# Kernel tuning notes

Hardware: AMD Instinct MI355X
Metric: run time of the kernel (lower is better)

Reference implementation:

```python
import jax, jax.numpy as jnp
import numpy as np

N_NODES = 50000
N_EDGES = 800000   # avg degree ~16
IN_CH = 128
HID = 64


def setup_inputs() -> dict:
    key = jax.random.key(0)
    k0, k1, k2, k3 = jax.random.split(key, 4)
    x = jax.random.normal(k0, (N_NODES, IN_CH), dtype=jnp.float32)
    edge_index = jax.random.randint(k1, (2, N_EDGES), 0, N_NODES, dtype=jnp.int32)
    # Glorot-ish init like torch GCNConv
    W1 = jax.random.normal(k2, (IN_CH, HID), dtype=jnp.float32) / np.sqrt(IN_CH).astype(np.float32)
    b1 = jnp.zeros((HID,), dtype=jnp.float32)
    W2 = jax.random.normal(k3, (HID, HID), dtype=jnp.float32) / np.sqrt(HID).astype(np.float32)
    b2 = jnpp = jnp.zeros((HID,), dtype=jnp.float32)
    return {"x": x, "edge_index": edge_index, "W1": W1, "b1": b1, "W2": W2, "b2": b2}


def gcn_conv(x, src, dst, W, b, n):
    """GCNConv with self-loops already appended to (src, dst).
    out = D^{-1/2} (A + I) D^{-1/2} (x @ W) + b, symmetric normalization."""
    h = x @ W                                        # [N, out]
    deg = jax.ops.segment_sum(jnp.ones(src.shape, jnp.float32), dst, num_segments=n)
    dinv = jax.lax.rsqrt(jnp.maximum(deg, 1.0))      # deg >= 1 due to self-loops
    norm = dinv[src] * dinv[dst]                     # [E+N]
    msg = h[src] * norm[:, None]                     # gather + scale
    return jax.ops.segment_sum(msg, dst, num_segments=n) + b


def reference(x, edge_index, W1, b1, W2, b2):
    n = x.shape[0]
    loop = jnp.arange(n, dtype=edge_index.dtype)
    src = jnp.concatenate([edge_index[0], loop])     # add self-loops
    dst = jnp.concatenate([edge_index[1], loop])
    # encode: GCNConv -> ReLU -> GCNConv
    z = jax.nn.relu(gcn_conv(x, src, dst, W1, b1, n))
    z = gcn_conv(z, src, dst, W2, b2, n)
    # decode: gather endpoint embeddings, elementwise product, reduce over hidden
    return (z[edge_index[0]] * z[edge_index[1]]).sum(axis=1)   # [E]
```

## Files before the change

kernel.cpp:

```cpp
#include <hip/hip_runtime.h>
#include <hip/hip_fp16.h>

#define INCH 128
#define HIDC 64
#define CAP  64

typedef int            v4i __attribute__((ext_vector_type(4)));
typedef float          v4f __attribute__((ext_vector_type(4)));
typedef float          v2f __attribute__((ext_vector_type(2)));
typedef unsigned int   v4u __attribute__((ext_vector_type(4)));

__device__ inline float2 u2f(unsigned int u) {
    return __half22float2(__builtin_bit_cast(__half2, u));
}
__device__ inline unsigned int f2u(float a, float b) {
    __half2 h = __float22half2_rn(make_float2(a, b));
    return __builtin_bit_cast(unsigned int, h);
}

__global__ __launch_bounds__(128, 2) void build_gemm1_kernel(const int* __restrict__ src,
                                                             const int* __restrict__ dst,
                                                             int* __restrict__ count,
                                                             unsigned short* __restrict__ col,
                                                             const float* __restrict__ x,
                                                             const float* __restrict__ W,
                                                             __half* __restrict__ hs,
                                                             int E, int N, int EB) {
    int b = (int)blockIdx.x;
    if (b < EB) {
        int i8 = (b * 128 + (int)threadIdx.x) * 8;
        if (i8 + 7 < E) {
            v4i sa = __builtin_nontemporal_load((const v4i*)(src + i8));
            v4i sb = __builtin_nontemporal_load((const v4i*)(src + i8 + 4));
            v4i da = __builtin_nontemporal_load((const v4i*)(dst + i8));
            v4i db = __builtin_nontemporal_load((const v4i*)(dst + i8 + 4));
            int rs[8], ds[8], ss[8];
            ds[0]=da.x; ds[1]=da.y; ds[2]=da.z; ds[3]=da.w;
            ds[4]=db.x; ds[5]=db.y; ds[6]=db.z; ds[7]=db.w;
            ss[0]=sa.x; ss[1]=sa.y; ss[2]=sa.z; ss[3]=sa.w;
            ss[4]=sb.x; ss[5]=sb.y; ss[6]=sb.z; ss[7]=sb.w;
            #pragma unroll
            for (int k = 0; k < 8; ++k) rs[k] = atomicAdd(&count[ds[k]], 1);
            #pragma unroll
            for (int k = 0; k < 8; ++k)
                if (rs[k] < CAP) col[ds[k] * CAP + rs[k]] = (unsigned short)ss[k];
        } else {
            for (int i = i8; i < E; ++i) {
                int d = dst[i];
                int r = atomicAdd(&count[d], 1);
                if (r < CAP) col[d * CAP + r] = (unsigned short)src[i];
            }
        }
    } else {
        int nb = b - EB;
        int node = (nb >> 1) * 128 + (int)threadIdx.x;
        int ch0 = (nb & 1) * 32;
        if (node >= N) return;
        const float4* xr = (const float4*)(x + (size_t)node * INCH);
        float acc[32];
        #pragma unroll
        for (int c = 0; c < 32; ++c) acc[c] = 0.f;
        for (int kc = 0; kc < INCH / 4; ++kc) {
            float4 xk = xr[kc];
            const float* wr = W + (kc * 4) * HIDC + ch0;
            #pragma unroll
            for (int ch = 0; ch < 32; ++ch) acc[ch] = fmaf(xk.x, wr[ch], acc[ch]);
            #pragma unroll
            for (int ch = 0; ch < 32; ++ch) acc[ch] = fmaf(xk.y, wr[HIDC + ch], acc[ch]);
            #pragma unroll
            for (int ch = 0; ch < 32; ++ch) acc[ch] = fmaf(xk.z, wr[2 * HIDC + ch], acc[ch]);
            #pragma unroll
            for (int ch = 0; ch < 32; ++ch) acc[ch] = fmaf(xk.w, wr[3 * HIDC + ch], acc[ch]);
        }
        v4u hv[4];
        #pragma unroll
        for (int k = 0; k < 4; ++k) {
            #pragma unroll
            for (int e = 0; e < 4; ++e) {
                int c2 = k * 4 + e;
                hv[k][e] = f2u(acc[2 * c2], acc[2 * c2 + 1]);
            }
        }
        v4u* hr = (v4u*)(hs + (size_t)node * HIDC + ch0);
        #pragma unroll
        for (int k = 0; k < 4; ++k) hr[k] = hv[k];
    }
}

__global__ __launch_bounds__(256) void scale_kernel(const int* __restrict__ count,
                                                    __half* __restrict__ hs, int N) {
    int idx = (int)blockIdx.x * 256 + threadIdx.x;
    if (idx >= N * 8) return;
    int node = idx >> 3;
    float dn = rsqrtf((float)count[node] + 1.0f);
    v4u v = ((const v4u*)hs)[idx];
    v4u o;
    #pragma unroll
    for (int k = 0; k < 4; ++k) {
        float2 f = u2f(v[k]);
        o[k] = f2u(dn * f.x, dn * f.y);
    }
    ((v4u*)hs)[idx] = o;
}

__global__ __launch_bounds__(128, 2) void gemm2_kernel(const __half* __restrict__ agg1,
                                                       const float* __restrict__ W,
                                                       const int* __restrict__ count,
                                                       __half* __restrict__ hs, int N) {
    int node = (blockIdx.x >> 1) * 128 + threadIdx.x;
    int ch0 = (blockIdx.x & 1) * 32;
    if (node >= N) return;
    const v4u* ar = (const v4u*)(agg1 + (size_t)node * HIDC);
    float acc[32];
    #pragma unroll
    for (int c = 0; c < 32; ++c) acc[c] = 0.f;
    for (int kc = 0; kc < HIDC / 8; ++kc) {
        v4u av = ar[kc];
        #pragma unroll
        for (int k2 = 0; k2 < 4; ++k2) {
            float2 f = u2f(av[k2]);
            float v0 = fmaxf(f.x, 0.f);
            float v1 = fmaxf(f.y, 0.f);
            const float* wr = W + (kc * 8 + k2 * 2) * HIDC + ch0;
            #pragma unroll
            for (int ch = 0; ch < 32; ++ch) acc[ch] = fmaf(v0, wr[ch], acc[ch]);
            #pragma unroll
            for (int ch = 0; ch < 32; ++ch) acc[ch] = fmaf(v1, wr[HIDC + ch], acc[ch]);
        }
    }
    float dn = rsqrtf((float)count[node] + 1.0f);
    v4u hv[4];
    #pragma unroll
    for (int k = 0; k < 4; ++k) {
        #pragma unroll
        for (int e = 0; e < 4; ++e) {
            int c2 = k * 4 + e;
            hv[k][e] = f2u(dn * acc[2 * c2], dn * acc[2 * c2 + 1]);
        }
    }
    v4u* hr = (v4u*)(hs + (size_t)node * HIDC + ch0);
    #pragma unroll
    for (int k = 0; k < 4; ++k) hr[k] = hv[k];
}

__global__ __launch_bounds__(256) void aggregate_kernel(const int* __restrict__ count,
                                                        const unsigned short* __restrict__ col,
                                                        const __half* __restrict__ hs,
                                                        const float* __restrict__ bias,
                                                        __half* __restrict__ agg, int N) {
    int node = blockIdx.x * 8 + (threadIdx.x >> 5);
    int c2 = threadIdx.x & 31;
    if (node >= N) return;
    int cnt = count[node];
    int deg = cnt < CAP ? cnt : CAP;
    const unsigned int* h2p = (const unsigned int*)hs;
    float2 acc = u2f(h2p[(size_t)node * 32 + c2]);
    const unsigned short* row = col + (size_t)node * CAP;
    for (int jb = 0; jb < deg; jb += 16) {
        int s[16];
        unsigned int v[16];
        #pragma unroll
        for (int u = 0; u < 16; ++u) {
            int idx = jb + u;
            s[u] = row[idx < deg ? idx : jb];
        }
        #pragma unroll
        for (int u = 0; u < 16; ++u)
            v[u] = h2p[(size_t)s[u] * 32 + c2];
        #pragma unroll
        for (int u = 0; u < 16; ++u) {
            if (jb + u < deg) {
                float2 f = u2f(v[u]);
                acc.x += f.x; acc.y += f.y;
            }
        }
    }
    float dn = rsqrtf((float)cnt + 1.0f);
    float2 bb = *(const float2*)(bias + c2 * 2);
    ((unsigned int*)agg)[(size_t)node * 32 + c2] =
        f2u(fmaf(acc.x, dn, bb.x), fmaf(acc.y, dn, bb.y));
}

__global__ __launch_bounds__(256) void decode_kernel(const int* __restrict__ src,
                                                     const int* __restrict__ dst,
                                                     const __half* __restrict__ z,
                                                     float* __restrict__ out, int E) {
    long long tid = (long long)blockIdx.x * 256 + threadIdx.x;
    int g = (int)(tid >> 3);
    int q = threadIdx.x & 7;
    int e0 = g * 4;
    if (e0 >= E) return;
    const v4u* z8 = (const v4u*)z;
    bool full = (e0 + 3 < E);
    int s[4], d[4];
    if (full) {
        v4i sv = __builtin_nontemporal_load((const v4i*)(src + e0));
        v4i dv = __builtin_nontemporal_load((const v4i*)(dst + e0));
        s[0]=sv.x; s[1]=sv.y; s[2]=sv.z; s[3]=sv.w;
        d[0]=dv.x; d[1]=dv.y; d[2]=dv.z; d[3]=dv.w;
    } else {
        #pragma unroll
        for (int k = 0; k < 4; ++k) {
            int e = e0 + k < E ? e0 + k : e0;
            s[k] = src[e]; d[k] = dst[e];
        }
    }
    v4u a[4], b[4];
    #pragma unroll
    for (int k = 0; k < 4; ++k) a[k] = z8[(size_t)s[k] * 8 + q];
    #pragma unroll
    for (int k = 0; k < 4; ++k) b[k] = z8[(size_t)d[k] * 8 + q];
    float p[4];
    #pragma unroll
    for (int k = 0; k < 4; ++k) {
        float acc = 0.f;
        #pragma unroll
        for (int j = 0; j < 4; ++j) {
            float2 fa = u2f(a[k][j]);
            float2 fb = u2f(b[k][j]);
            acc = fmaf(fa.x, fb.x, acc);
            acc = fmaf(fa.y, fb.y, acc);
        }
        p[k] = acc;
    }
    #pragma unroll
    for (int m = 4; m; m >>= 1) {
        #pragma unroll
        for (int k = 0; k < 4; ++k) p[k] += __shfl_xor(p[k], m, 64);
    }
    if (q == 0) {
        if (full) {
            v4f r; r.x = p[0]; r.y = p[1]; r.z = p[2]; r.w = p[3];
            __builtin_nontemporal_store(r, (v4f*)(out + e0));
        } else {
            for (int k = 0; k < 4 && e0 + k < E; ++k) out[e0 + k] = p[k];
        }
    }
}

extern "C" void kernel_launch(void* const* d_in, const int* in_sizes, int n_in,
                              void* d_out, int out_size, void* d_ws, size_t ws_size,
                              hipStream_t stream) {
    const float* x  = (const float*)d_in[0];
    const int*   ei = (const int*)d_in[1];
    const float* W1 = (const float*)d_in[2];
    const float* b1 = (const float*)d_in[3];
    const float* W2 = (const float*)d_in[4];
    const float* b2 = (const float*)d_in[5];
    float* out = (float*)d_out;

    const int hid  = in_sizes[3];
    const int inch = in_sizes[2] / hid;
    const int N    = in_sizes[0] / inch;
    const int E    = in_sizes[1] / 2;
    const int* srcp = ei;
    const int* dstp = ei + E;

    char* p = (char*)d_ws;
    auto alloc = [&](size_t bytes) { char* r = p; p += (bytes + 255) & ~(size_t)255; return r; };
    int*            count = (int*)alloc((size_t)N * 4);
    unsigned short* col   = (unsigned short*)alloc((size_t)N * CAP * 2);
    __half*         h1s   = (__half*)alloc((size_t)N * HIDC * 2);
    __half*         h2s   = (__half*)alloc((size_t)N * HIDC * 2);
    __half*         zt    = (__half*)alloc((size_t)N * HIDC * 2);
    __half*         agg1  = (__half*)alloc((size_t)N * HIDC * 2);

    (void)hipMemsetAsync(count, 0, (size_t)N * 4, stream);

    int EB = (E / 8 + 127) / 128 + 1;
    int GB = 2 * ((N + 127) / 128);
    build_gemm1_kernel<<<EB + GB, 128, 0, stream>>>(srcp, dstp, count, col,
                                                    x, W1, h1s, E, N, EB);
    scale_kernel<<<(N * 8 + 255) / 256, 256, 0, stream>>>(count, h1s, N);

    aggregate_kernel<<<(N + 7) / 8, 256, 0, stream>>>(count, col, h1s, b1, agg1, N);
    gemm2_kernel<<<GB, 128, 0, stream>>>(agg1, W2, count, h2s, N);
    aggregate_kernel<<<(N + 7) / 8, 256, 0, stream>>>(count, col, h2s, b2, zt, N);

    long long groups = ((long long)E + 3) / 4;
    long long blocksD = (groups * 8 + 255) / 256;
    decode_kernel<<<(int)blocksD, 256, 0, stream>>>(srcp, dstp, zt, out, E);
}
```

Baseline: 212.5 us.

## Partition CSR build edges by destination residue across eight block groups

The edge-bucketing part of the fused build/GEMM1 kernel now uses groups of 8 blocks per 2048-edge chunk. Each block in a group reads the whole chunk but only inserts edges whose destination mod 8 matches its group id, which spreads atomics and column writes across blocks by destination. The GEMM blocks are also placed first in the grid so the compute work starts earlier. The cost is 8x redundant reads of src/dst, and the nontemporal loads are replaced by plain loads.

```diff
diff --git a/kernel.cpp b/kernel.cpp
--- a/kernel.cpp
+++ b/kernel.cpp
@@ -25,36 +25,48 @@
                                                              const float* __restrict__ x,
                                                              const float* __restrict__ W,
                                                              __half* __restrict__ hs,
-                                                             int E, int N, int EB) {
+                                                             int E, int N, int GB) {
     int b = (int)blockIdx.x;
-    if (b < EB) {
-        int i8 = (b * 128 + (int)threadIdx.x) * 8;
-        if (i8 + 7 < E) {
-            v4i sa = __builtin_nontemporal_load((const v4i*)(src + i8));
-            v4i sb = __builtin_nontemporal_load((const v4i*)(src + i8 + 4));
-            v4i da = __builtin_nontemporal_load((const v4i*)(dst + i8));
-            v4i db = __builtin_nontemporal_load((const v4i*)(dst + i8 + 4));
-            int rs[8], ds[8], ss[8];
-            ds[0]=da.x; ds[1]=da.y; ds[2]=da.z; ds[3]=da.w;
-            ds[4]=db.x; ds[5]=db.y; ds[6]=db.z; ds[7]=db.w;
-            ss[0]=sa.x; ss[1]=sa.y; ss[2]=sa.z; ss[3]=sa.w;
-            ss[4]=sb.x; ss[5]=sb.y; ss[6]=sb.z; ss[7]=sb.w;
-            #pragma unroll
-            for (int k = 0; k < 8; ++k) rs[k] = atomicAdd(&count[ds[k]], 1);
-            #pragma unroll
-            for (int k = 0; k < 8; ++k)
-                if (rs[k] < CAP) col[ds[k] * CAP + rs[k]] = (unsigned short)ss[k];
+    if (b >= GB) {
+        int eb = b - GB;
+        int g = eb & 7;
+        int chunkBase = (eb >> 3) * 2048;
+        int t = (int)threadIdx.x;
+        if (chunkBase + 2048 <= E) {
+            v4i s4[4], d4[4];
+            #pragma unroll
+            for (int i = 0; i < 4; ++i) {
+                int e0 = chunkBase + (i * 128 + t) * 4;
+                d4[i] = *(const v4i*)(dst + e0);
+                s4[i] = *(const v4i*)(src + e0);
+            }
+            #pragma unroll
+            for (int i = 0; i < 4; ++i) {
+                #pragma unroll
+                for (int k = 0; k < 4; ++k) {
+                    int d = d4[i][k];
+                    if ((d & 7) == g) {
+                        int r = atomicAdd(&count[d], 1);
+                        if (r < CAP) col[(size_t)d * CAP + r] = (unsigned short)s4[i][k];
+                    }
+                }
+            }
         } else {
-            for (int i = i8; i < E; ++i) {
-                int d = dst[i];
-                int r = atomicAdd(&count[d], 1);
-                if (r < CAP) col[d * CAP + r] = (unsigned short)src[i];
+            #pragma unroll
+            for (int i = 0; i < 4; ++i) {
+                int e0 = chunkBase + (i * 128 + t) * 4;
+                for (int e = e0; e < e0 + 4 && e < E; ++e) {
+                    int d = dst[e];
+                    if ((d & 7) == g) {
+                        int r = atomicAdd(&count[d], 1);
+                        if (r < CAP) col[(size_t)d * CAP + r] = (unsigned short)src[e];
+                    }
+                }
             }
         }
     } else {
-        int nb = b - EB;
-        int node = (nb >> 1) * 128 + (int)threadIdx.x;
-        int ch0 = (nb & 1) * 32;
+        int node = (b >> 1) * 128 + (int)threadIdx.x;
+        int ch0 = (b & 1) * 32;
         if (node >= N) return;
         const float4* xr = (const float4*)(x + (size_t)node * INCH);
         float acc[32];
@@ -267,10 +279,10 @@
 
     (void)hipMemsetAsync(count, 0, (size_t)N * 4, stream);
 
-    int EB = (E / 8 + 127) / 128 + 1;
-    int GB = 2 * ((N + 127) / 128);
-    build_gemm1_kernel<<<EB + GB, 128, 0, stream>>>(srcp, dstp, count, col,
-                                                    x, W1, h1s, E, N, EB);
+    int GB  = 2 * ((N + 127) / 128);
+    int EBK = 8 * ((E + 2047) / 2048);
+    build_gemm1_kernel<<<GB + EBK, 128, 0, stream>>>(srcp, dstp, count, col,
+                                                     x, W1, h1s, E, N, GB);
     scale_kernel<<<(N * 8 + 255) / 256, 256, 0, stream>>>(count, h1s, N);
 
     aggregate_kernel<<<(N + 7) / 8, 256, 0, stream>>>(count, col, h1s, b1, agg1, N);
```

Measured after the change: 204.2 us. 1.04x faster.

## Build CSR per node-range in shared memory and fuse degree scaling into GEMM1

Applied to the files above, without the earlier changes.

Adjacency construction moves from global atomics on random destination nodes to per-block LDS bucketing. Each block owns 448 destination nodes, scans the whole edge list, and writes its count and column slab out contiguously. This removes the count memset and the separate scale kernel, and folds the D^-1/2 scaling into gemm1's epilogue. The cost is that every block rereads the full dst array, about 112 blocks on a much larger GPU. Build and gemm1 also no longer overlap in one launch.

```diff
diff --git a/kernel.cpp b/kernel.cpp
--- a/kernel.cpp
+++ b/kernel.cpp
@@ -4,10 +4,10 @@
 #define INCH 128
 #define HIDC 64
 #define CAP  64
+#define RNODES 448
 
 typedef int            v4i __attribute__((ext_vector_type(4)));
 typedef float          v4f __attribute__((ext_vector_type(4)));
-typedef float          v2f __attribute__((ext_vector_type(2)));
 typedef unsigned int   v4u __attribute__((ext_vector_type(4)));
 
 __device__ inline float2 u2f(unsigned int u) {
@@ -18,89 +18,94 @@
     return __builtin_bit_cast(unsigned int, h);
 }
 
-__global__ __launch_bounds__(128, 2) void build_gemm1_kernel(const int* __restrict__ src,
-                                                             const int* __restrict__ dst,
-                                                             int* __restrict__ count,
-                                                             unsigned short* __restrict__ col,
-                                                             const float* __restrict__ x,
-                                                             const float* __restrict__ W,
-                                                             __half* __restrict__ hs,
-                                                             int E, int N, int EB) {
-    int b = (int)blockIdx.x;
-    if (b < EB) {
-        int i8 = (b * 128 + (int)threadIdx.x) * 8;
-        if (i8 + 7 < E) {
-            v4i sa = __builtin_nontemporal_load((const v4i*)(src + i8));
-            v4i sb = __builtin_nontemporal_load((const v4i*)(src + i8 + 4));
-            v4i da = __builtin_nontemporal_load((const v4i*)(dst + i8));
-            v4i db = __builtin_nontemporal_load((const v4i*)(dst + i8 + 4));
-            int rs[8], ds[8], ss[8];
-            ds[0]=da.x; ds[1]=da.y; ds[2]=da.z; ds[3]=da.w;
-            ds[4]=db.x; ds[5]=db.y; ds[6]=db.z; ds[7]=db.w;
-            ss[0]=sa.x; ss[1]=sa.y; ss[2]=sa.z; ss[3]=sa.w;
-            ss[4]=sb.x; ss[5]=sb.y; ss[6]=sb.z; ss[7]=sb.w;
+__global__ __launch_bounds__(512) void build_kernel(const int* __restrict__ src,
+                                                    const int* __restrict__ dst,
+                                                    int* __restrict__ count,
+                                                    unsigned short* __restrict__ col,
+                                                    int E, int N) {
+    __shared__ int lcnt[RNODES];
+    __shared__ unsigned short lcol[RNODES * CAP];
+    int n0 = (int)blockIdx.x * RNODES;
+    int t = (int)threadIdx.x;
+    for (int i = t; i < RNODES; i += 512) lcnt[i] = 0;
+    __syncthreads();
+
+    for (int base = t * 8; base < E; base += 512 * 8) {
+        if (base + 8 <= E) {
+            v4i da = *(const v4i*)(dst + base);
+            v4i db = *(const v4i*)(dst + base + 4);
+            int d[8];
+            d[0]=da.x; d[1]=da.y; d[2]=da.z; d[3]=da.w;
+            d[4]=db.x; d[5]=db.y; d[6]=db.z; d[7]=db.w;
             #pragma unroll
-            for (int k = 0; k < 8; ++k) rs[k] = atomicAdd(&count[ds[k]], 1);
-            #pragma unroll
-            for (int k = 0; k < 8; ++k)
-                if (rs[k] < CAP) col[ds[k] * CAP + rs[k]] = (unsigned short)ss[k];
+            for (int k = 0; k < 8; ++k) {
+                unsigned r = (unsigned)(d[k] - n0);
+                if (r < RNODES) {
+                    int s = src[base + k];
+                    int slot = atomicAdd(&lcnt[r], 1);
+                    if (slot < CAP) lcol[r * CAP + slot] = (unsigned short)s;
+                }
+            }
         } else {
-            for (int i = i8; i < E; ++i) {
-                int d = dst[i];
-                int r = atomicAdd(&count[d], 1);
-                if (r < CAP) col[d * CAP + r] = (unsigned short)src[i];
+            for (int e = base; e < E; ++e) {
+                unsigned r = (unsigned)(dst[e] - n0);
+                if (r < RNODES) {
+                    int s = src[e];
+                    int slot = atomicAdd(&lcnt[r], 1);
+                    if (slot < CAP) lcol[r * CAP + slot] = (unsigned short)s;
+                }
             }
         }
-    } else {
-        int nb = b - EB;
-        int node = (nb >> 1) * 128 + (int)threadIdx.x;
-        int ch0 = (nb & 1) * 32;
-        if (node >= N) return;
-        const float4* xr = (const float4*)(x + (size_t)node * INCH);
-        float acc[32];
-        #pragma unroll
-        for (int c = 0; c < 32; ++c) acc[c] = 0.f;
-        for (int kc = 0; kc < INCH / 4; ++kc) {
-            float4 xk = xr[kc];
-            const float* wr = W + (kc * 4) * HIDC + ch0;
-            #pragma unroll
-            for (int ch = 0; ch < 32; ++ch) acc[ch] = fmaf(xk.x, wr[ch], acc[ch]);
-            #pragma unroll
-            for (int ch = 0; ch < 32; ++ch) acc[ch] = fmaf(xk.y, wr[HIDC + ch], acc[ch]);
-            #pragma unroll
-            for (int ch = 0; ch < 32; ++ch) acc[ch] = fmaf(xk.z, wr[2 * HIDC + ch], acc[ch]);
-            #pragma unroll
-            for (int ch = 0; ch < 32; ++ch) acc[ch] = fmaf(xk.w, wr[3 * HIDC + ch], acc[ch]);
-        }
-        v4u hv[4];
-        #pragma unroll
-        for (int k = 0; k < 4; ++k) {
-            #pragma unroll
-            for (int e = 0; e < 4; ++e) {
-                int c2 = k * 4 + e;
-                hv[k][e] = f2u(acc[2 * c2], acc[2 * c2 + 1]);
-            }
-        }
-        v4u* hr = (v4u*)(hs + (size_t)node * HIDC + ch0);
-        #pragma unroll
-        for (int k = 0; k < 4; ++k) hr[k] = hv[k];
-    }
-}
-
-__global__ __launch_bounds__(256) void scale_kernel(const int* __restrict__ count,
-                                                    __half* __restrict__ hs, int N) {
-    int idx = (int)blockIdx.x * 256 + threadIdx.x;
-    if (idx >= N * 8) return;
-    int node = idx >> 3;
+    }
+    __syncthreads();
+
+    for (int i = t; i < RNODES; i += 512) {
+        int n = n0 + i;
+        if (n < N) count[n] = lcnt[i];
+    }
+    const v4u* lp = (const v4u*)lcol;
+    for (int i = t; i < RNODES * 8; i += 512) {
+        int n = n0 + (i >> 3);
+        if (n < N) ((v4u*)col)[(size_t)n * 8 + (i & 7)] = lp[i];
+    }
+}
+
+__global__ __launch_bounds__(128, 2) void gemm1_kernel(const float* __restrict__ x,
+                                                       const float* __restrict__ W,
+                                                       const int* __restrict__ count,
+                                                       __half* __restrict__ hs, int N) {
+    int node = ((int)blockIdx.x >> 1) * 128 + (int)threadIdx.x;
+    int ch0 = ((int)blockIdx.x & 1) * 32;
+    if (node >= N) return;
+    const float4* xr = (const float4*)(x + (size_t)node * INCH);
+    float acc[32];
+    #pragma unroll
+    for (int c = 0; c < 32; ++c) acc[c] = 0.f;
+    for (int kc = 0; kc < INCH / 4; ++kc) {
+        float4 xk = xr[kc];
+        const float* wr = W + (kc * 4) * HIDC + ch0;
+        #pragma unroll
+        for (int ch = 0; ch < 32; ++ch) acc[ch] = fmaf(xk.x, wr[ch], acc[ch]);
+        #pragma unroll
+        for (int ch = 0; ch < 32; ++ch) acc[ch] = fmaf(xk.y, wr[HIDC + ch], acc[ch]);
+        #pragma unroll
+        for (int ch = 0; ch < 32; ++ch) acc[ch] = fmaf(xk.z, wr[2 * HIDC + ch], acc[ch]);
+        #pragma unroll
+        for (int ch = 0; ch < 32; ++ch) acc[ch] = fmaf(xk.w, wr[3 * HIDC + ch], acc[ch]);
+    }
     float dn = rsqrtf((float)count[node] + 1.0f);
-    v4u v = ((const v4u*)hs)[idx];
-    v4u o;
+    v4u hv[4];
     #pragma unroll
     for (int k = 0; k < 4; ++k) {
-        float2 f = u2f(v[k]);
-        o[k] = f2u(dn * f.x, dn * f.y);
-    }
-    ((v4u*)hs)[idx] = o;
+        #pragma unroll
+        for (int e = 0; e < 4; ++e) {
+            int c2 = k * 4 + e;
+            hv[k][e] = f2u(dn * acc[2 * c2], dn * acc[2 * c2 + 1]);
+        }
+    }
+    v4u* hr = (v4u*)(hs + (size_t)node * HIDC + ch0);
+    #pragma unroll
+    for (int k = 0; k < 4; ++k) hr[k] = hv[k];
 }
 
 __global__ __launch_bounds__(128, 2) void gemm2_kernel(const __half* __restrict__ agg1,
@@ -265,13 +270,11 @@
     __half*         zt    = (__half*)alloc((size_t)N * HIDC * 2);
     __half*         agg1  = (__half*)alloc((size_t)N * HIDC * 2);
 
-    (void)hipMemsetAsync(count, 0, (size_t)N * 4, stream);
-
-    int EB = (E / 8 + 127) / 128 + 1;
+    int BB = (N + RNODES - 1) / RNODES;
+    build_kernel<<<BB, 512, 0, stream>>>(srcp, dstp, count, col, E, N);
+
     int GB = 2 * ((N + 127) / 128);
-    build_gemm1_kernel<<<EB + GB, 128, 0, stream>>>(srcp, dstp, count, col,
-                                                    x, W1, h1s, E, N, EB);
-    scale_kernel<<<(N * 8 + 255) / 256, 256, 0, stream>>>(count, h1s, N);
+    gemm1_kernel<<<GB, 128, 0, stream>>>(x, W1, count, h1s, N);
 
     aggregate_kernel<<<(N + 7) / 8, 256, 0, stream>>>(count, col, h1s, b1, agg1, N);
     gemm2_kernel<<<GB, 128, 0, stream>>>(agg1, W2, count, h2s, N);
```

After: 437.6 us. +105.9%, slower.
